# Kernel tuning notes

Hardware: AMD Instinct MI355X
Metric: run time of the kernel (lower is better)

The kernel has to match this reference:

```python
import jax, jax.numpy as jnp
import numpy as np

EPS = 0.3          # FAGCN eps residual coefficient
N_LAYERS = 2


def setup_inputs() -> dict:
    key = jax.random.key(0)
    ks = jax.random.split(key, 8)
    N, E, IN, H, OUT = 50000, 800000, 256, 64, 16
    return {
        "h": jax.random.normal(ks[0], (N, IN), dtype=jnp.float32),
        "src": jax.random.randint(ks[1], (E,), 0, N, dtype=jnp.int32),
        "dst": jax.random.randint(ks[2], (E,), 0, N, dtype=jnp.int32),
        "t1_w": jax.random.normal(ks[3], (H, IN), dtype=jnp.float32) * (1.414 / np.sqrt(IN)),
        "t1_b": jnp.zeros((H,), dtype=jnp.float32),
        "gate_w": jax.random.normal(ks[4], (N_LAYERS, 2 * H), dtype=jnp.float32) * (1.414 / np.sqrt(2 * H)),
        "gate_b": jnp.zeros((N_LAYERS,), dtype=jnp.float32),
        "t2_w": jax.random.normal(ks[5], (OUT, H), dtype=jnp.float32) * (1.414 / np.sqrt(H)),
        "t2_b": jnp.zeros((OUT,), dtype=jnp.float32),
    }


def reference(h, src, dst, t1_w, t1_b, gate_w, gate_b, t2_w, t2_b):
    N = h.shape[0]
    # symmetric degree norm d = in_degree^-0.5 (as in FAGCN preprocessing)
    deg = jnp.zeros((N,), dtype=h.dtype).at[dst].add(1.0)
    d = jax.lax.rsqrt(jnp.maximum(deg, 1.0))

    # t1 + relu (dropout is identity in eval mode)
    x = jax.nn.relu(h @ t1_w.T + t1_b)          # [N, H]
    raw = x
    for l in range(N_LAYERS):
        hs = x[src]                              # [E, H] gathered src feats
        hd = x[dst]                              # [E, H] gathered dst feats
        # gate(concat[dst, src]) -> tanh -> scalar per edge
        g = jnp.tanh(jnp.concatenate([hd, hs], axis=-1) @ gate_w[l] + gate_b[l])  # [E]
        e = g * d[dst] * d[src]                  # [E]
        msg = hs * e[:, None]                    # [E, H]
        z = jax.ops.segment_sum(msg, dst, num_segments=N)  # scatter-sum to dst
        x = EPS * raw + z

    logits = x @ t2_w.T + t2_b                   # [N, OUT]
    return jax.nn.log_softmax(logits, axis=-1)
```

## Files before the change

kernel.cpp:

```cpp
#include <hip/hip_runtime.h>
#include <math.h>

#define EPS 0.3f

typedef __attribute__((ext_vector_type(8))) short bf16x8;
typedef __attribute__((ext_vector_type(4))) float f32x4;

__device__ __forceinline__ short f2bf(float f) {
    union { float f; unsigned u; } v; v.f = f;
    unsigned r = v.u + 0x7FFFu + ((v.u >> 16) & 1u);
    return (short)(r >> 16);
}
__device__ __forceinline__ float bf2f(short s) {
    union { unsigned u; float f; } v;
    v.u = ((unsigned)(unsigned short)s) << 16;
    return v.f;
}
__device__ __forceinline__ int f2bf_pk(float lo, float hi) {
#if __has_builtin(__builtin_amdgcn_cvt_pk_bf16_f32)
    auto r = __builtin_amdgcn_cvt_pk_bf16_f32(lo, hi);
    int out; __builtin_memcpy(&out, &r, 4);
    return out;
#else
    return ((int)(unsigned short)f2bf(lo)) | (((int)(unsigned short)f2bf(hi)) << 16);
#endif
}
__device__ __forceinline__ float fast_tanh(float x) {
    return 1.0f - 2.0f / (1.0f + __expf(2.0f * x));
}


__global__ __launch_bounds__(256) void coarse_hist(const int* __restrict__ dst,
                                                   int* __restrict__ hist2d, int E,
                                                   const float* __restrict__ w,
                                                   short* __restrict__ wb) {
    if (blockIdx.x < 64) {
        int i = blockIdx.x * 256 + threadIdx.x;
        wb[i] = f2bf(w[i]);
    }
    __shared__ int lh[256];
    lh[threadIdx.x] = 0;
    __syncthreads();
    for (int i = blockIdx.x * 256 + threadIdx.x; i < E; i += gridDim.x * 256)
        atomicAdd(&lh[dst[i] >> 8], 1);
    __syncthreads();
    hist2d[blockIdx.x * 256 + threadIdx.x] = lh[threadIdx.x];
}

__global__ void coarse_scan(const int* __restrict__ hist2d, int* __restrict__ cbase,
                            int* __restrict__ ccur, int* __restrict__ rs,
                            int NBIN, int N, int E) {
    __shared__ int tmp[256];
    int tid = threadIdx.x;
    int v = 0;
    #pragma unroll 8
    for (int b = 0; b < 256; ++b) v += hist2d[b * 256 + tid];
    if (tid >= NBIN) v = 0;
    tmp[tid] = v;
    __syncthreads();
    #pragma unroll
    for (int off = 1; off < 256; off <<= 1) {
        int o = (tid >= off) ? tmp[tid - off] : 0;
        __syncthreads();
        tmp[tid] += o;
        __syncthreads();
    }
    if (tid < NBIN) { cbase[tid] = tmp[tid] - v; ccur[tid] = tmp[tid] - v; }
    if (tid == NBIN - 1) cbase[NBIN] = tmp[tid];
    if (tid == 0) rs[N] = E;
}

__global__ __launch_bounds__(256) void partition(const int* __restrict__ src,
                                                 const int* __restrict__ dst,
                                                 int* __restrict__ ccur,
                                                 unsigned* __restrict__ part, int E) {
    __shared__ int lh[256];
    __shared__ int lbase[256];
    int tid = threadIdx.x;
    int chunk = (E + gridDim.x - 1) / gridDim.x;
    int s0 = blockIdx.x * chunk;
    int s1 = min(s0 + chunk, E);
    lh[tid] = 0;
    __syncthreads();
    for (int i = s0 + tid; i < s1; i += 256) atomicAdd(&lh[dst[i] >> 8], 1);
    __syncthreads();
    int c = lh[tid];
    lbase[tid] = c ? atomicAdd(&ccur[tid], c) : 0;
    __syncthreads();
    lh[tid] = 0;
    __syncthreads();
    for (int i = s0 + tid; i < s1; i += 256) {
        int t = dst[i];
        int b = t >> 8;
        int r = atomicAdd(&lh[b], 1);
        part[lbase[b] + r] = (unsigned)src[i] | ((unsigned)(t & 255) << 16);
    }
}

#define LROW 264
__global__ __launch_bounds__(256) void csr_t1(
    const unsigned* __restrict__ part, const int* __restrict__ cbase,
    int* __restrict__ rs, unsigned short* __restrict__ esrc,
    const float* __restrict__ h, const short* __restrict__ wb,
    const float* __restrict__ t1b, const float* __restrict__ gw,
    short* __restrict__ XAh, float* __restrict__ ga0,
    float* __restrict__ bd0f, float* __restrict__ bd1f, int N, int NBIN)
{
    __shared__ short lds[4][16 * LROW];
    int tid = threadIdx.x;

    if ((int)blockIdx.x < NBIN) {
        int* lcnt = (int*)&lds[0][0];
        int* s    = lcnt + 256;
        int* lcur = s + 256;
        int t0 = blockIdx.x << 8;
        int e0 = cbase[blockIdx.x], e1 = cbase[blockIdx.x + 1];
        lcnt[tid] = 0;
        __syncthreads();
        for (int i = e0 + tid; i < e1; i += 256) atomicAdd(&lcnt[(part[i] >> 16) & 255], 1);
        __syncthreads();
        int v = lcnt[tid];
        s[tid] = v;
        __syncthreads();
        #pragma unroll
        for (int off = 1; off < 256; off <<= 1) {
            int o = (tid >= off) ? s[tid - off] : 0;
            __syncthreads();
            s[tid] += o;
            __syncthreads();
        }
        int excl = s[tid] - v;
        int node = t0 + tid;
        if (node < N) {
            rs[node] = e0 + excl;
            float dval = rsqrtf(fmaxf((float)v, 1.0f));
            bd0f[2 * node + 1] = dval;
            bd1f[2 * node + 1] = dval;
        }
        lcur[tid] = e0 + excl;
        __syncthreads();
        for (int i = e0 + tid; i < e1; i += 256) {
            unsigned e = part[i];
            int slot = atomicAdd(&lcur[(e >> 16) & 255], 1);
            esrc[slot] = (unsigned short)(e & 0xFFFFu);
        }
        return;
    }

    int bid = blockIdx.x - NBIN;
    int wave = tid >> 6;
    int lane = tid & 63;
    int l15 = lane & 15, quad = lane >> 4;
    int M0 = (bid * 4 + wave) * 16;
    if (M0 >= N) return;
    int rlim = N - M0;

    short* myl = lds[wave];
    const float* hb = h + (size_t)M0 * 256;
    #pragma unroll
    for (int r = 0; r < 16; ++r) {
        if (r < rlim) {
            float4 v = *(const float4*)&hb[(size_t)r * 256 + lane * 4];
            int2 sv; sv.x = f2bf_pk(v.x, v.y); sv.y = f2bf_pk(v.z, v.w);
            *(int2*)&myl[r * LROW + lane * 4] = sv;
        }
    }

    f32x4 acc[4];
    #pragma unroll
    for (int nt = 0; nt < 4; ++nt) acc[nt] = (f32x4){0.f, 0.f, 0.f, 0.f};

    const short* wq = wb + quad * 8;
    #pragma unroll
    for (int kc = 0; kc < 256; kc += 32) {
        bf16x8 af = *(const bf16x8*)&myl[l15 * LROW + kc + quad * 8];
        #pragma unroll
        for (int nt = 0; nt < 4; ++nt) {
            bf16x8 bf = *(const bf16x8*)(wq + (size_t)(nt * 16 + l15) * 256 + kc);
            acc[nt] = __builtin_amdgcn_mfma_f32_16x16x32_bf16(af, bf, acc[nt], 0, 0, 0);
        }
    }

    float pa[4] = {0.f, 0.f, 0.f, 0.f};
    float pb[4] = {0.f, 0.f, 0.f, 0.f};
    #pragma unroll
    for (int nt = 0; nt < 4; ++nt) {
        int n = nt * 16 + l15;
        float bias = t1b[n];
        float gd = gw[n], gs = gw[64 + n];
        #pragma unroll
        for (int r = 0; r < 4; ++r) {
            int row = quad * 4 + r;
            if (row < rlim) {
                float x = fmaxf(acc[nt][r] + bias, 0.f);
                XAh[(size_t)(M0 + row) * 64 + n] = f2bf(x);
                pa[r] += x * gd;
                pb[r] += x * gs;
            }
        }
    }
    #pragma unroll
    for (int off = 1; off < 16; off <<= 1) {
        #pragma unroll
        for (int r = 0; r < 4; ++r) {
            pa[r] += __shfl_xor(pa[r], off, 64);
            pb[r] += __shfl_xor(pb[r], off, 64);
        }
    }
    if (l15 == 0) {
        #pragma unroll
        for (int r = 0; r < 4; ++r) {
            int row = quad * 4 + r;
            if (row < rlim) {
                ga0[M0 + row] = pa[r];
                bd0f[2 * (M0 + row)] = pb[r];
            }
        }
    }
}

__device__ __forceinline__ void gather_core2(
    const int* __restrict__ rs, const unsigned short* __restrict__ esrc,
    const float* __restrict__ a, const float2* __restrict__ bd,
    const short* __restrict__ xch, const short* __restrict__ rawh,
    float gbias, int t, int lane, float acc[8])
{
    int g = (lane >> 3) & 3;
    int l = lane & 7;
    int j = lane & 31;
    int hbase = lane & 32;

    int beg = rs[t], end = rs[t + 1];
    int deg = end - beg;
    float atg = a[t] + gbias;
    float dt = bd[t].y;

    int ev = (j < deg) ? (int)esrc[beg + j] : 0;
    float2 bde = bd[ev];
    float cv = fast_tanh(atg + bde.x) * dt * bde.y;

    int sarr[8]; float carr[8];
    #pragma unroll
    for (int k = 0; k < 8; ++k) {
        int srcl = hbase + g + 4 * k;
        sarr[k] = __shfl(ev, srcl, 64);
        carr[k] = __shfl(cv, srcl, 64);
    }

    #pragma unroll
    for (int k = 0; k < 8; ++k) acc[k] = 0.f;
    if (g == 0) {
        bf16x8 rv = *(const bf16x8*)&rawh[(size_t)t * 64 + l * 8];
        #pragma unroll
        for (int k = 0; k < 8; ++k) acc[k] = EPS * bf2f(rv[k]);
    }

    int lim = min(deg, 32);
    #pragma unroll
    for (int k = 0; k < 8; ++k) {
        if (g + 4 * k < lim) {
            int s0 = sarr[k];
            float c0 = carr[k];
            bf16x8 x0 = *(const bf16x8*)&xch[(size_t)s0 * 64 + l * 8];
            #pragma unroll
            for (int kk = 0; kk < 8; ++kk) acc[kk] += c0 * bf2f(x0[kk]);
        }
    }
    for (int i = beg + 32 + g; i < end; i += 4) {
        int s0 = (int)esrc[i];
        float2 bd0 = bd[s0];
        bf16x8 x0 = *(const bf16x8*)&xch[(size_t)s0 * 64 + l * 8];
        float c0 = fast_tanh(atg + bd0.x) * dt * bd0.y;
        #pragma unroll
        for (int k = 0; k < 8; ++k) acc[k] += c0 * bf2f(x0[k]);
    }

    #pragma unroll
    for (int off = 8; off < 32; off <<= 1) {
        #pragma unroll
        for (int k = 0; k < 8; ++k) acc[k] += __shfl_xor(acc[k], off, 64);
    }
}

__global__ __launch_bounds__(256) void gather_mid(
    const int* __restrict__ rs, const unsigned short* __restrict__ esrc,
    const float* __restrict__ a, const float2* __restrict__ bd,
    const short* __restrict__ xch, const float* __restrict__ gbp,
    short* __restrict__ xnh, const float* __restrict__ gw_next,
    float* __restrict__ ga_next, float* __restrict__ bd_next_f, int N)
{
    int tid = threadIdx.x;
    int t = blockIdx.x * 8 + (tid >> 5);
    int tt = min(t, N - 1);
    bool valid = (t < N);
    int lane = tid & 63;
    int g = (lane >> 3) & 3, l = lane & 7;
    float acc[8];
    gather_core2(rs, esrc, a, bd, xch, xch, gbp[0], tt, lane, acc);

    if (g == 0 && valid) {
        int4 o;
        o.x = f2bf_pk(acc[0], acc[1]); o.y = f2bf_pk(acc[2], acc[3]);
        o.z = f2bf_pk(acc[4], acc[5]); o.w = f2bf_pk(acc[6], acc[7]);
        *(int4*)&xnh[(size_t)tt * 64 + l * 8] = o;
    }
    float av = 0.f, bv = 0.f;
    #pragma unroll
    for (int k = 0; k < 8; ++k) {
        av += acc[k] * gw_next[l * 8 + k];
        bv += acc[k] * gw_next[64 + l * 8 + k];
    }
    #pragma unroll
    for (int off = 1; off < 8; off <<= 1) {
        av += __shfl_xor(av, off, 64);
        bv += __shfl_xor(bv, off, 64);
    }
    if ((lane & 31) == 0 && valid) {
        ga_next[tt] = av;
        bd_next_f[2 * tt] = bv;
    }
}

__global__ __launch_bounds__(256) void gather_out(
    const int* __restrict__ rs, const unsigned short* __restrict__ esrc,
    const float* __restrict__ a, const float2* __restrict__ bd,
    const short* __restrict__ xch, const short* __restrict__ rawh,
    const float* __restrict__ gbp, const float* __restrict__ t2w,
    const float* __restrict__ t2b, float* __restrict__ out, int N)
{
    int tid = threadIdx.x;
    int t = blockIdx.x * 8 + (tid >> 5);
    int tt = min(t, N - 1);
    bool valid = (t < N);
    int lane = tid & 63;
    int g = (lane >> 3) & 3, l = lane & 7;
    float acc[8];
    gather_core2(rs, esrc, a, bd, xch, rawh, gbp[1], tt, lane, acc);

    int j0 = 4 * g;
    float p[4];
    #pragma unroll
    for (int i = 0; i < 4; ++i) {
        const float* w = &t2w[(size_t)(j0 + i) * 64 + l * 8];
        float s = 0.f;
        #pragma unroll
        for (int k = 0; k < 8; ++k) s += acc[k] * w[k];
        p[i] = s;
    }
    #pragma unroll
    for (int off = 1; off < 8; off <<= 1) {
        #pragma unroll
        for (int i = 0; i < 4; ++i) p[i] += __shfl_xor(p[i], off, 64);
    }
    float li[4];
    #pragma unroll
    for (int i = 0; i < 4; ++i) li[i] = p[i] + t2b[j0 + i];
    float m = fmaxf(fmaxf(li[0], li[1]), fmaxf(li[2], li[3]));
    #pragma unroll
    for (int off = 8; off < 32; off <<= 1) m = fmaxf(m, __shfl_xor(m, off, 64));
    float s = 0.f;
    #pragma unroll
    for (int i = 0; i < 4; ++i) s += __expf(li[i] - m);
    #pragma unroll
    for (int off = 8; off < 32; off <<= 1) s += __shfl_xor(s, off, 64);
    float lse = m + __logf(s);
    if (l == 0 && valid) {
        float4 o;
        o.x = li[0] - lse; o.y = li[1] - lse;
        o.z = li[2] - lse; o.w = li[3] - lse;
        *(float4*)&out[(size_t)tt * 16 + j0] = o;
    }
}

extern "C" void kernel_launch(void* const* d_in, const int* in_sizes, int n_in,
                              void* d_out, int out_size, void* d_ws, size_t ws_size,
                              hipStream_t stream) {
    const float* h    = (const float*)d_in[0];
    const int*   src  = (const int*)d_in[1];
    const int*   dst  = (const int*)d_in[2];
    const float* t1w  = (const float*)d_in[3];
    const float* t1b  = (const float*)d_in[4];
    const float* gw   = (const float*)d_in[5];
    const float* gbia = (const float*)d_in[6];
    const float* t2w  = (const float*)d_in[7];
    const float* t2b  = (const float*)d_in[8];
    float* out = (float*)d_out;

    int N = in_sizes[0] / 256;
    int E = in_sizes[1];
    int NBIN = (N + 255) / 256;

    char* p = (char*)d_ws;
    short*    XAh    = (short*)p;       p += (size_t)N * 64 * 2;
    short*    XBh    = (short*)p;       p += (size_t)N * 64 * 2;
    float*    ga0    = (float*)p;       p += (size_t)N * 4;
    float*    ga1    = (float*)p;       p += (size_t)N * 4;
    float2*   bd0    = (float2*)p;      p += (size_t)N * 8;
    float2*   bd1    = (float2*)p;      p += (size_t)N * 8;
    int*      rs     = (int*)p;         p += (size_t)(N + 1) * 4;
    int*      hist2d = (int*)p;         p += 256 * 256 * 4;
    int*      cbase  = (int*)p;         p += 257 * 4;
    int*      ccur   = (int*)p;         p += 256 * 4;
    p = (char*)(((size_t)p + 15) & ~(size_t)15);
    unsigned* part   = (unsigned*)p;    p += (size_t)E * 4;
    unsigned short* esrc = (unsigned short*)p; p += (size_t)E * 2;
    p = (char*)(((size_t)p + 15) & ~(size_t)15);
    short*    wbf    = (short*)p;

    coarse_hist<<<256, 256, 0, stream>>>(dst, hist2d, E, t1w, wbf);
    coarse_scan<<<1, 256, 0, stream>>>(hist2d, cbase, ccur, rs, NBIN, N, E);
    partition<<<256, 256, 0, stream>>>(src, dst, ccur, part, E);

    csr_t1<<<NBIN + (N + 63) / 64, 256, 0, stream>>>(
        part, cbase, rs, esrc, h, wbf, t1b, gw, XAh, ga0,
        (float*)bd0, (float*)bd1, N, NBIN);

    gather_mid<<<(N + 7) / 8, 256, 0, stream>>>(rs, esrc, ga0, bd0, XAh, gbia,
                                                XBh, gw + 128, ga1, (float*)bd1, N);

    gather_out<<<(N + 7) / 8, 256, 0, stream>>>(rs, esrc, ga1, bd1, XBh, XAh, gbia,
                                                t2w, t2b, out, N);
}
```

Before: 200.7 us.

## Replace sorted CSR build with fixed-capacity per-node atomic bucket scatter

Drops the histogram, scan and partition kernels that built a sorted CSR, and instead scatters each edge's source into a fixed 64-slot row per destination node using a global atomic counter, with an overflow spill list. Degree normalisation is now computed on the fly from the counters, and the scatter blocks share a launch with the t1 GEMM blocks. This removes three launches and two passes over the edge arrays, in exchange for random global atomics, non-deterministic neighbor order, a larger padded index buffer, and a spill scan in the gather whenever overflow occurs. Spill entries beyond the cap would be silently lost.

```diff
diff --git a/kernel.cpp b/kernel.cpp
--- a/kernel.cpp
+++ b/kernel.cpp
@@ -2,6 +2,8 @@
 #include <math.h>
 
 #define EPS 0.3f
+#define CAP 64
+#define SPILLCAP 65536
 
 typedef __attribute__((ext_vector_type(8))) short bf16x8;
 typedef __attribute__((ext_vector_type(4))) float f32x4;
@@ -30,124 +32,45 @@
 }
 
 
-__global__ __launch_bounds__(256) void coarse_hist(const int* __restrict__ dst,
-                                                   int* __restrict__ hist2d, int E,
-                                                   const float* __restrict__ w,
-                                                   short* __restrict__ wb) {
-    if (blockIdx.x < 64) {
-        int i = blockIdx.x * 256 + threadIdx.x;
-        wb[i] = f2bf(w[i]);
-    }
-    __shared__ int lh[256];
-    lh[threadIdx.x] = 0;
-    __syncthreads();
-    for (int i = blockIdx.x * 256 + threadIdx.x; i < E; i += gridDim.x * 256)
-        atomicAdd(&lh[dst[i] >> 8], 1);
-    __syncthreads();
-    hist2d[blockIdx.x * 256 + threadIdx.x] = lh[threadIdx.x];
-}
-
-__global__ void coarse_scan(const int* __restrict__ hist2d, int* __restrict__ cbase,
-                            int* __restrict__ ccur, int* __restrict__ rs,
-                            int NBIN, int N, int E) {
-    __shared__ int tmp[256];
-    int tid = threadIdx.x;
-    int v = 0;
-    #pragma unroll 8
-    for (int b = 0; b < 256; ++b) v += hist2d[b * 256 + tid];
-    if (tid >= NBIN) v = 0;
-    tmp[tid] = v;
-    __syncthreads();
-    #pragma unroll
-    for (int off = 1; off < 256; off <<= 1) {
-        int o = (tid >= off) ? tmp[tid - off] : 0;
-        __syncthreads();
-        tmp[tid] += o;
-        __syncthreads();
-    }
-    if (tid < NBIN) { cbase[tid] = tmp[tid] - v; ccur[tid] = tmp[tid] - v; }
-    if (tid == NBIN - 1) cbase[NBIN] = tmp[tid];
-    if (tid == 0) rs[N] = E;
-}
-
-__global__ __launch_bounds__(256) void partition(const int* __restrict__ src,
-                                                 const int* __restrict__ dst,
-                                                 int* __restrict__ ccur,
-                                                 unsigned* __restrict__ part, int E) {
-    __shared__ int lh[256];
-    __shared__ int lbase[256];
-    int tid = threadIdx.x;
-    int chunk = (E + gridDim.x - 1) / gridDim.x;
-    int s0 = blockIdx.x * chunk;
-    int s1 = min(s0 + chunk, E);
-    lh[tid] = 0;
-    __syncthreads();
-    for (int i = s0 + tid; i < s1; i += 256) atomicAdd(&lh[dst[i] >> 8], 1);
-    __syncthreads();
-    int c = lh[tid];
-    lbase[tid] = c ? atomicAdd(&ccur[tid], c) : 0;
-    __syncthreads();
-    lh[tid] = 0;
-    __syncthreads();
-    for (int i = s0 + tid; i < s1; i += 256) {
-        int t = dst[i];
-        int b = t >> 8;
-        int r = atomicAdd(&lh[b], 1);
-        part[lbase[b] + r] = (unsigned)src[i] | ((unsigned)(t & 255) << 16);
-    }
+__global__ __launch_bounds__(256) void init_k(const float* __restrict__ w,
+                                              short* __restrict__ wb,
+                                              int* __restrict__ cnt,
+                                              int* __restrict__ spillN, int N) {
+    int bid = blockIdx.x, tid = threadIdx.x;
+    if (bid < 64) wb[bid * 256 + tid] = f2bf(w[bid * 256 + tid]);
+    for (int i = bid * 256 + tid; i < N; i += gridDim.x * 256) cnt[i] = 0;
+    if (bid == 0 && tid == 0) *spillN = 0;
 }
 
 #define LROW 264
-__global__ __launch_bounds__(256) void csr_t1(
-    const unsigned* __restrict__ part, const int* __restrict__ cbase,
-    int* __restrict__ rs, unsigned short* __restrict__ esrc,
+__global__ __launch_bounds__(256) void scatter_t1(
+    const int* __restrict__ src, const int* __restrict__ dst, int E,
+    int* __restrict__ cnt, unsigned short* __restrict__ esrc2,
+    unsigned* __restrict__ spill, int* __restrict__ spillN,
     const float* __restrict__ h, const short* __restrict__ wb,
     const float* __restrict__ t1b, const float* __restrict__ gw,
-    short* __restrict__ XAh, float* __restrict__ ga0,
-    float* __restrict__ bd0f, float* __restrict__ bd1f, int N, int NBIN)
+    short* __restrict__ XAh, float* __restrict__ ga0, float* __restrict__ gb0,
+    int N, int SCB)
 {
     __shared__ short lds[4][16 * LROW];
     int tid = threadIdx.x;
 
-    if ((int)blockIdx.x < NBIN) {
-        int* lcnt = (int*)&lds[0][0];
-        int* s    = lcnt + 256;
-        int* lcur = s + 256;
-        int t0 = blockIdx.x << 8;
-        int e0 = cbase[blockIdx.x], e1 = cbase[blockIdx.x + 1];
-        lcnt[tid] = 0;
-        __syncthreads();
-        for (int i = e0 + tid; i < e1; i += 256) atomicAdd(&lcnt[(part[i] >> 16) & 255], 1);
-        __syncthreads();
-        int v = lcnt[tid];
-        s[tid] = v;
-        __syncthreads();
-        #pragma unroll
-        for (int off = 1; off < 256; off <<= 1) {
-            int o = (tid >= off) ? s[tid - off] : 0;
-            __syncthreads();
-            s[tid] += o;
-            __syncthreads();
-        }
-        int excl = s[tid] - v;
-        int node = t0 + tid;
-        if (node < N) {
-            rs[node] = e0 + excl;
-            float dval = rsqrtf(fmaxf((float)v, 1.0f));
-            bd0f[2 * node + 1] = dval;
-            bd1f[2 * node + 1] = dval;
-        }
-        lcur[tid] = e0 + excl;
-        __syncthreads();
-        for (int i = e0 + tid; i < e1; i += 256) {
-            unsigned e = part[i];
-            int slot = atomicAdd(&lcur[(e >> 16) & 255], 1);
-            esrc[slot] = (unsigned short)(e & 0xFFFFu);
+    if ((int)blockIdx.x < SCB) {
+        for (int i = blockIdx.x * 256 + tid; i < E; i += SCB * 256) {
+            int d = dst[i];
+            int slot = atomicAdd(&cnt[d], 1);
+            if (slot < CAP) {
+                esrc2[(size_t)d * CAP + slot] = (unsigned short)src[i];
+            } else {
+                int sp = atomicAdd(spillN, 1);
+                if (sp < SPILLCAP)
+                    spill[sp] = ((unsigned)d << 16) | (unsigned)(src[i] & 0xFFFF);
+            }
         }
         return;
     }
 
-    int bid = blockIdx.x - NBIN;
+    int bid = blockIdx.x - SCB;
     int wave = tid >> 6;
     int lane = tid & 63;
     int l15 = lane & 15, quad = lane >> 4;
@@ -213,15 +136,16 @@
             int row = quad * 4 + r;
             if (row < rlim) {
                 ga0[M0 + row] = pa[r];
-                bd0f[2 * (M0 + row)] = pb[r];
+                gb0[M0 + row] = pb[r];
             }
         }
     }
 }
 
-__device__ __forceinline__ void gather_core2(
-    const int* __restrict__ rs, const unsigned short* __restrict__ esrc,
-    const float* __restrict__ a, const float2* __restrict__ bd,
+__device__ __forceinline__ void gather_core3(
+    const int* __restrict__ cnt, const unsigned short* __restrict__ esrc2,
+    const float* __restrict__ a, const float* __restrict__ gb,
+    const unsigned* __restrict__ spill, const int* __restrict__ spillN,
     const short* __restrict__ xch, const short* __restrict__ rawh,
     float gbias, int t, int lane, float acc[8])
 {
@@ -230,14 +154,16 @@
     int j = lane & 31;
     int hbase = lane & 32;
 
-    int beg = rs[t], end = rs[t + 1];
-    int deg = end - beg;
+    int deg = cnt[t];
+    int degrow = min(deg, CAP);
+    int beg = t * CAP;
     float atg = a[t] + gbias;
-    float dt = bd[t].y;
-
-    int ev = (j < deg) ? (int)esrc[beg + j] : 0;
-    float2 bde = bd[ev];
-    float cv = fast_tanh(atg + bde.x) * dt * bde.y;
+    float dt = rsqrtf(fmaxf((float)deg, 1.0f));
+
+    int ev = (j < degrow) ? (int)esrc2[beg + j] : 0;
+    float gbe = gb[ev];
+    float ce = (float)cnt[ev];
+    float cv = fast_tanh(atg + gbe) * dt * rsqrtf(fmaxf(ce, 1.0f));
 
     int sarr[8]; float carr[8];
     #pragma unroll
@@ -255,7 +181,7 @@
         for (int k = 0; k < 8; ++k) acc[k] = EPS * bf2f(rv[k]);
     }
 
-    int lim = min(deg, 32);
+    int lim = min(degrow, 32);
     #pragma unroll
     for (int k = 0; k < 8; ++k) {
         if (g + 4 * k < lim) {
@@ -266,14 +192,26 @@
             for (int kk = 0; kk < 8; ++kk) acc[kk] += c0 * bf2f(x0[kk]);
         }
     }
-    for (int i = beg + 32 + g; i < end; i += 4) {
-        int s0 = (int)esrc[i];
-        float2 bd0 = bd[s0];
+    for (int i = beg + 32 + g; i < beg + degrow; i += 4) {
+        int s0 = (int)esrc2[i];
+        float c0 = fast_tanh(atg + gb[s0]) * dt * rsqrtf(fmaxf((float)cnt[s0], 1.f));
         bf16x8 x0 = *(const bf16x8*)&xch[(size_t)s0 * 64 + l * 8];
-        float c0 = fast_tanh(atg + bd0.x) * dt * bd0.y;
         #pragma unroll
         for (int k = 0; k < 8; ++k) acc[k] += c0 * bf2f(x0[k]);
     }
+    int sn = min(*spillN, SPILLCAP);
+    if (sn > 0) {
+        for (int i = 0; i < sn; ++i) {
+            unsigned e = spill[i];
+            if ((int)(e >> 16) == t && g == 0) {
+                int s0 = (int)(e & 0xFFFFu);
+                float c0 = fast_tanh(atg + gb[s0]) * dt * rsqrtf(fmaxf((float)cnt[s0], 1.f));
+                bf16x8 x0 = *(const bf16x8*)&xch[(size_t)s0 * 64 + l * 8];
+                #pragma unroll
+                for (int k = 0; k < 8; ++k) acc[k] += c0 * bf2f(x0[k]);
+            }
+        }
+    }
 
     #pragma unroll
     for (int off = 8; off < 32; off <<= 1) {
@@ -283,11 +221,12 @@
 }
 
 __global__ __launch_bounds__(256) void gather_mid(
-    const int* __restrict__ rs, const unsigned short* __restrict__ esrc,
-    const float* __restrict__ a, const float2* __restrict__ bd,
+    const int* __restrict__ cnt, const unsigned short* __restrict__ esrc2,
+    const float* __restrict__ a, const float* __restrict__ gb,
+    const unsigned* __restrict__ spill, const int* __restrict__ spillN,
     const short* __restrict__ xch, const float* __restrict__ gbp,
     short* __restrict__ xnh, const float* __restrict__ gw_next,
-    float* __restrict__ ga_next, float* __restrict__ bd_next_f, int N)
+    float* __restrict__ ga_next, float* __restrict__ gb_next, int N)
 {
     int tid = threadIdx.x;
     int t = blockIdx.x * 8 + (tid >> 5);
@@ -296,7 +235,7 @@
     int lane = tid & 63;
     int g = (lane >> 3) & 3, l = lane & 7;
     float acc[8];
-    gather_core2(rs, esrc, a, bd, xch, xch, gbp[0], tt, lane, acc);
+    gather_core3(cnt, esrc2, a, gb, spill, spillN, xch, xch, gbp[0], tt, lane, acc);
 
     if (g == 0 && valid) {
         int4 o;
@@ -317,13 +256,14 @@
     }
     if ((lane & 31) == 0 && valid) {
         ga_next[tt] = av;
-        bd_next_f[2 * tt] = bv;
+        gb_next[tt] = bv;
     }
 }
 
 __global__ __launch_bounds__(256) void gather_out(
-    const int* __restrict__ rs, const unsigned short* __restrict__ esrc,
-    const float* __restrict__ a, const float2* __restrict__ bd,
+    const int* __restrict__ cnt, const unsigned short* __restrict__ esrc2,
+    const float* __restrict__ a, const float* __restrict__ gb,
+    const unsigned* __restrict__ spill, const int* __restrict__ spillN,
     const short* __restrict__ xch, const short* __restrict__ rawh,
     const float* __restrict__ gbp, const float* __restrict__ t2w,
     const float* __restrict__ t2b, float* __restrict__ out, int N)
@@ -335,7 +275,7 @@
     int lane = tid & 63;
     int g = (lane >> 3) & 3, l = lane & 7;
     float acc[8];
-    gather_core2(rs, esrc, a, bd, xch, rawh, gbp[1], tt, lane, acc);
+    gather_core3(cnt, esrc2, a, gb, spill, spillN, xch, rawh, gbp[1], tt, lane, acc);
 
     int j0 = 4 * g;
     float p[4];
@@ -388,36 +328,32 @@
 
     int N = in_sizes[0] / 256;
     int E = in_sizes[1];
-    int NBIN = (N + 255) / 256;
 
     char* p = (char*)d_ws;
     short*    XAh    = (short*)p;       p += (size_t)N * 64 * 2;
     short*    XBh    = (short*)p;       p += (size_t)N * 64 * 2;
     float*    ga0    = (float*)p;       p += (size_t)N * 4;
     float*    ga1    = (float*)p;       p += (size_t)N * 4;
-    float2*   bd0    = (float2*)p;      p += (size_t)N * 8;
-    float2*   bd1    = (float2*)p;      p += (size_t)N * 8;
-    int*      rs     = (int*)p;         p += (size_t)(N + 1) * 4;
-    int*      hist2d = (int*)p;         p += 256 * 256 * 4;
-    int*      cbase  = (int*)p;         p += 257 * 4;
-    int*      ccur   = (int*)p;         p += 256 * 4;
+    float*    gb0    = (float*)p;       p += (size_t)N * 4;
+    float*    gb1    = (float*)p;       p += (size_t)N * 4;
+    int*      cnt    = (int*)p;         p += (size_t)N * 4;
+    int*      spillN = (int*)p;         p += 16;
+    unsigned* spill  = (unsigned*)p;    p += (size_t)SPILLCAP * 4;
     p = (char*)(((size_t)p + 15) & ~(size_t)15);
-    unsigned* part   = (unsigned*)p;    p += (size_t)E * 4;
-    unsigned short* esrc = (unsigned short*)p; p += (size_t)E * 2;
+    unsigned short* esrc2 = (unsigned short*)p; p += (size_t)N * CAP * 2;
     p = (char*)(((size_t)p + 15) & ~(size_t)15);
     short*    wbf    = (short*)p;
 
-    coarse_hist<<<256, 256, 0, stream>>>(dst, hist2d, E, t1w, wbf);
-    coarse_scan<<<1, 256, 0, stream>>>(hist2d, cbase, ccur, rs, NBIN, N, E);
-    partition<<<256, 256, 0, stream>>>(src, dst, ccur, part, E);
-
-    csr_t1<<<NBIN + (N + 63) / 64, 256, 0, stream>>>(
-        part, cbase, rs, esrc, h, wbf, t1b, gw, XAh, ga0,
-        (float*)bd0, (float*)bd1, N, NBIN);
-
-    gather_mid<<<(N + 7) / 8, 256, 0, stream>>>(rs, esrc, ga0, bd0, XAh, gbia,
-                                                XBh, gw + 128, ga1, (float*)bd1, N);
-
-    gather_out<<<(N + 7) / 8, 256, 0, stream>>>(rs, esrc, ga1, bd1, XBh, XAh, gbia,
-                                                t2w, t2b, out, N);
-}
+    init_k<<<256, 256, 0, stream>>>(t1w, wbf, cnt, spillN, N);
+
+    int SCB = 240;
+    scatter_t1<<<SCB + (N + 63) / 64, 256, 0, stream>>>(
+        src, dst, E, cnt, esrc2, spill, spillN,
+        h, wbf, t1b, gw, XAh, ga0, gb0, N, SCB);
+
+    gather_mid<<<(N + 7) / 8, 256, 0, stream>>>(cnt, esrc2, ga0, gb0, spill, spillN,
+                                                XAh, gbia, XBh, gw + 128, ga1, gb1, N);
+
+    gather_out<<<(N + 7) / 8, 256, 0, stream>>>(cnt, esrc2, ga1, gb1, spill, spillN,
+                                                XBh, XAh, gbia, t2w, t2b, out, N);
+}
```

Result: slower. 205.4 us (+2.3%).
